# Optimization experiments

Measured on AMD Instinct MI355X. Metric: run time of the kernel, lower is better.

## Reference

```python
import jax, jax.numpy as jnp
import numpy as np

TAU = 0.5
EPS = 1e-8  # torch CosineSimilarity eps


def _normalize(v):
    # matches torch cosine sim: divide by max(||v||, eps)
    n = jnp.linalg.norm(v, axis=-1, keepdims=True)
    return v / jnp.maximum(n, EPS)


def setup_inputs() -> dict:
    key = jax.random.key(0)
    k1, k2 = jax.random.split(key)
    N, D = 4096, 256
    x = jax.random.normal(k1, (N, D), dtype=jnp.float32)
    y = jax.random.normal(k2, (N, D), dtype=jnp.float32)
    return {"x": x, "y": y}


def reference(x, y):
    n = x.shape[0]
    xn = _normalize(x)
    yn = _normalize(y)
    inv_tau = 1.0 / TAU
    sim_xx = (xn @ xn.T) * inv_tau  # [n, n]
    sim_yy = (yn @ yn.T) * inv_tau
    sim_xy = (xn @ yn.T) * inv_tau
    neg_inf = jnp.float32(-jnp.inf)
    diag = jnp.arange(n)
    sim_xx = sim_xx.at[diag, diag].set(neg_inf)
    sim_yy = sim_yy.at[diag, diag].set(neg_inf)
    scores1 = jnp.concatenate([sim_xy, sim_xx], axis=-1)          # [n, 2n]
    scores2 = jnp.concatenate([sim_yy, sim_xy.T], axis=-1)        # [n, 2n]
    scores = jnp.concatenate([scores1, scores2], axis=-2)          # [2n, 2n]
    targets = jnp.arange(2 * n)
    logp = jax.nn.log_softmax(scores, axis=-1)
    loss = -jnp.mean(logp[jnp.arange(2 * n), targets])
    return loss
```

## Files before the change

kernel.cpp:

```cpp
#include <hip/hip_runtime.h>
#include <hip/hip_bf16.h>


#define NROWS 8192
#define DDIM  256
#define BM    128
#define BN    64
#define COLSPLIT 8
#define COLS_PER (NROWS / COLSPLIT)
#define NT (COLS_PER / BN)

typedef __attribute__((ext_vector_type(8))) __bf16 bf16x8_t;
typedef __attribute__((ext_vector_type(4))) float  f32x4_t;

typedef __attribute__((address_space(1))) const void* as1_cvp;
typedef __attribute__((address_space(3))) void*       as3_vp;

#if __has_builtin(__builtin_amdgcn_exp2f)
#define EXP2F __builtin_amdgcn_exp2f
#else
#define EXP2F exp2f
#endif

#define TWO_LOG2E 2.8853900817779268f

__global__ __launch_bounds__(256) void normalize_diag_kernel(
    const float* __restrict__ x, const float* __restrict__ y,
    __hip_bfloat16* __restrict__ zb, float* __restrict__ rowdiag,
    float* __restrict__ rowsum) {
  const int g = blockIdx.x * 256 + threadIdx.x;
  if (g < NROWS) rowsum[g] = 0.f;

  const int w = threadIdx.x >> 6, lane = threadIdx.x & 63;
  const int i = blockIdx.x * 4 + w;
  const float4 xv = ((const float4*)(x + (size_t)i * DDIM))[lane];
  const float4 yv = ((const float4*)(y + (size_t)i * DDIM))[lane];
  float ssx = xv.x * xv.x + xv.y * xv.y + xv.z * xv.z + xv.w * xv.w;
  float ssy = yv.x * yv.x + yv.y * yv.y + yv.z * yv.z + yv.w * yv.w;
  float sxy = xv.x * yv.x + xv.y * yv.y + xv.z * yv.z + xv.w * yv.w;
  #pragma unroll
  for (int off = 32; off > 0; off >>= 1) {
    ssx += __shfl_xor(ssx, off, 64);
    ssy += __shfl_xor(ssy, off, 64);
    sxy += __shfl_xor(sxy, off, 64);
  }
  const float sclx = 1.0f / fmaxf(sqrtf(ssx), 1e-8f);
  const float scly = 1.0f / fmaxf(sqrtf(ssy), 1e-8f);
  __hip_bfloat16 px[4], py[4];
  px[0] = __float2bfloat16(xv.x * sclx); px[1] = __float2bfloat16(xv.y * sclx);
  px[2] = __float2bfloat16(xv.z * sclx); px[3] = __float2bfloat16(xv.w * sclx);
  py[0] = __float2bfloat16(yv.x * scly); py[1] = __float2bfloat16(yv.y * scly);
  py[2] = __float2bfloat16(yv.z * scly); py[3] = __float2bfloat16(yv.w * scly);
  *(short4*)(zb + (size_t)i * DDIM + lane * 4)            = *(short4*)px;
  *(short4*)(zb + (size_t)(i + 4096) * DDIM + lane * 4)   = *(short4*)py;
  if (lane == 0) rowdiag[i] = 2.0f * sxy * sclx * scly;
}

__global__ __launch_bounds__(512) void gram_lse_kernel(
    const __hip_bfloat16* __restrict__ zbh, float* __restrict__ rowsum) {
  __shared__ short smem[2][BN * DDIM];

  const short* zs = (const short*)zbh;
  const char* zbytes = (const char*)zs;
  const int tid  = threadIdx.x;
  const int w    = tid >> 6;
  const int lane = tid & 63;
  const int lhi  = lane >> 4;
  const int llo  = lane & 15;
  const int i0 = (blockIdx.x >> 3) * BM;
  const int c0 = (blockIdx.x & 7) * COLS_PER;
  const bool has_diag = ((blockIdx.x >> 6) == (blockIdx.x & 7));

  const int arow = i0 + w * 16 + llo;
  const float TBF = __bfloat162float(__float2bfloat16(TWO_LOG2E));
  bf16x8_t afrag[8];
  #pragma unroll
  for (int ks = 0; ks < 8; ++ks) {
    afrag[ks] = *(const bf16x8_t*)(zs + (size_t)arow * DDIM + ks * 32 + lhi * 8);
    #pragma unroll
    for (int e = 0; e < 8; ++e) {
      afrag[ks][e] = (__bf16)((float)afrag[ks][e] * TBF);
    }
  }

  size_t soff[4]; int loff[4];
  #pragma unroll
  for (int it = 0; it < 4; ++it) {
    const int o    = w * 4096 + it * 1024 + lane * 16;
    const int cr   = o >> 9;
    const int slot = (o >> 4) & 31;
    soff[it] = (size_t)cr * 512 + (size_t)((slot ^ (cr & 31)) << 4);
    loff[it] = w * 4096 + it * 1024;
  }

#define STAGE(buf, ct_) do {                                                  \
    const size_t cbase = (size_t)(c0 + (ct_) * BN) * 512;                     \
    _Pragma("unroll")                                                         \
    for (int it = 0; it < 4; ++it) {                                          \
      __builtin_amdgcn_global_load_lds(                                       \
          (as1_cvp)(zbytes + cbase + soff[it]),                               \
          (as3_vp)((char*)smem[buf] + loff[it]), 16, 0, 0);                   \
    }                                                                         \
  } while (0)

  float racc[4] = {0.f, 0.f, 0.f, 0.f};
  const int gr_base = i0 + w * 16 + lhi * 4;

  STAGE(0, 0);
  asm volatile("s_waitcnt vmcnt(0)" ::: "memory");
  __syncthreads();
  int cur = 0;

  for (int ct = 0; ct < NT; ++ct) {
    if (ct + 1 < NT) STAGE(cur ^ 1, ct + 1);
    const int cb = c0 + ct * BN;

    #pragma unroll
    for (int nt = 0; nt < 4; ++nt) {
      const int cr = nt * 16 + llo;
      f32x4_t acc = {0.f, 0.f, 0.f, 0.f};
      #pragma unroll
      for (int ks = 0; ks < 8; ++ks) {
        const int kg = ks * 4 + lhi;
        const bf16x8_t bfrag = *(const bf16x8_t*)(
            (const char*)smem[cur] + cr * 512 + ((kg ^ (cr & 31)) << 4));
        acc = __builtin_amdgcn_mfma_f32_16x16x32_bf16(afrag[ks], bfrag, acc, 0, 0, 0);
      }
      if (has_diag) {
        const int gc = cb + cr;
        #pragma unroll
        for (int j = 0; j < 4; ++j)
          racc[j] += ((gr_base + j) != gc) ? EXP2F(acc[j]) : 0.f;
      } else {
        #pragma unroll
        for (int j = 0; j < 4; ++j)
          racc[j] += EXP2F(acc[j]);
      }
    }
    asm volatile("s_waitcnt vmcnt(0)" ::: "memory");
    __syncthreads();
    cur ^= 1;
  }
#undef STAGE

  #pragma unroll
  for (int j = 0; j < 4; ++j) {
    float v = racc[j];
    v += __shfl_xor(v, 1, 16);
    v += __shfl_xor(v, 2, 16);
    v += __shfl_xor(v, 4, 16);
    v += __shfl_xor(v, 8, 16);
    if (llo == 0) atomicAdd(&rowsum[gr_base + j], v);
  }
}

__global__ __launch_bounds__(256) void finalize_kernel(
    const float* __restrict__ rowsum, const float* __restrict__ rowdiag,
    float* __restrict__ out) {
  const int t = threadIdx.x;
  float s = 0.f;
  for (int r4 = t; r4 < NROWS / 4; r4 += 256) {
    const float4 v = ((const float4*)rowsum)[r4];
    s += __logf(v.x) + __logf(v.y) + __logf(v.z) + __logf(v.w);
  }
  for (int i4 = t; i4 < 4096 / 4; i4 += 256) {
    const float4 d = ((const float4*)rowdiag)[i4];
    s -= 2.0f * (d.x + d.y + d.z + d.w);
  }
  #pragma unroll
  for (int off = 32; off > 0; off >>= 1) s += __shfl_xor(s, off, 64);
  __shared__ float wsum[4];
  const int w = t >> 6, lane = t & 63;
  if (lane == 0) wsum[w] = s;
  __syncthreads();
  if (t == 0) out[0] = (wsum[0] + wsum[1] + wsum[2] + wsum[3]) / (float)NROWS;
}

extern "C" void kernel_launch(void* const* d_in, const int* in_sizes, int n_in,
                              void* d_out, int out_size, void* d_ws, size_t ws_size,
                              hipStream_t stream) {
  const float* x = (const float*)d_in[0];
  const float* y = (const float*)d_in[1];
  float* out = (float*)d_out;

  char* ws = (char*)d_ws;
  __hip_bfloat16* zb = (__hip_bfloat16*)ws;
  float* rowsum  = (float*)(ws + (size_t)NROWS * DDIM * 2);
  float* rowdiag = rowsum + NROWS;

  normalize_diag_kernel<<<1024, 256, 0, stream>>>(x, y, zb, rowdiag, rowsum);
  gram_lse_kernel<<<512, 512, 0, stream>>>(zb, rowsum);
  finalize_kernel<<<1, 256, 0, stream>>>(rowsum, rowdiag, out);
}
```

Measured before the change: 55.35 us.

## Exploit Gram matrix symmetry by computing lower-triangular tiles only

```diff
diff --git a/kernel.cpp b/kernel.cpp
--- a/kernel.cpp
+++ b/kernel.cpp
@@ -6,9 +6,9 @@
 #define DDIM  256
 #define BM    128
 #define BN    64
-#define COLSPLIT 8
-#define COLS_PER (NROWS / COLSPLIT)
+#define COLS_PER 256
 #define NT (COLS_PER / BN)
+#define NBLK 1056
 
 typedef __attribute__((ext_vector_type(8))) __bf16 bf16x8_t;
 typedef __attribute__((ext_vector_type(4))) float  f32x4_t;
@@ -58,7 +58,8 @@
 
 __global__ __launch_bounds__(512) void gram_lse_kernel(
     const __hip_bfloat16* __restrict__ zbh, float* __restrict__ rowsum) {
-  __shared__ short smem[2][BN * DDIM];
+  __shared__ short smem[BN * DDIM];
+  __shared__ float colacc[COLS_PER];
 
   const short* zs = (const short*)zbh;
   const char* zbytes = (const char*)zs;
@@ -67,9 +68,15 @@
   const int lane = tid & 63;
   const int lhi  = lane >> 4;
   const int llo  = lane & 15;
-  const int i0 = (blockIdx.x >> 3) * BM;
-  const int c0 = (blockIdx.x & 7) * COLS_PER;
-  const bool has_diag = ((blockIdx.x >> 6) == (blockIdx.x & 7));
+
+  int jj = 0, rem = blockIdx.x;
+  while (rem >= 64 - 2 * jj) { rem -= 64 - 2 * jj; ++jj; }
+  const int I = 2 * jj + rem;
+  const int i0 = I * BM;
+  const int c0 = jj * COLS_PER;
+  const bool straddle = (rem <= 1);
+
+  if (tid < COLS_PER) colacc[tid] = 0.f;
 
   const int arow = i0 + w * 16 + llo;
   const float TBF = __bfloat162float(__float2bfloat16(TWO_LOG2E));
@@ -78,42 +85,36 @@
   for (int ks = 0; ks < 8; ++ks) {
     afrag[ks] = *(const bf16x8_t*)(zs + (size_t)arow * DDIM + ks * 32 + lhi * 8);
     #pragma unroll
-    for (int e = 0; e < 8; ++e) {
+    for (int e = 0; e < 8; ++e)
       afrag[ks][e] = (__bf16)((float)afrag[ks][e] * TBF);
-    }
   }
 
-  size_t soff[4]; int loff[4];
+  int soff[4], loff[4];
   #pragma unroll
   for (int it = 0; it < 4; ++it) {
-    const int o    = w * 4096 + it * 1024 + lane * 16;
+    const int o    = it * 8192 + tid * 16;
     const int cr   = o >> 9;
     const int slot = (o >> 4) & 31;
-    soff[it] = (size_t)cr * 512 + (size_t)((slot ^ (cr & 31)) << 4);
-    loff[it] = w * 4096 + it * 1024;
+    soff[it] = cr * 512 + ((slot ^ (cr & 31)) << 4);
+    loff[it] = it * 8192 + w * 1024;
   }
 
-#define STAGE(buf, ct_) do {                                                  \
-    const size_t cbase = (size_t)(c0 + (ct_) * BN) * 512;                     \
-    _Pragma("unroll")                                                         \
-    for (int it = 0; it < 4; ++it) {                                          \
-      __builtin_amdgcn_global_load_lds(                                       \
-          (as1_cvp)(zbytes + cbase + soff[it]),                               \
-          (as3_vp)((char*)smem[buf] + loff[it]), 16, 0, 0);                   \
-    }                                                                         \
-  } while (0)
-
   float racc[4] = {0.f, 0.f, 0.f, 0.f};
-  const int gr_base = i0 + w * 16 + lhi * 4;
-
-  STAGE(0, 0);
-  asm volatile("s_waitcnt vmcnt(0)" ::: "memory");
-  __syncthreads();
-  int cur = 0;
+  const int gr0 = i0 + w * 16 + lhi * 4;
 
   for (int ct = 0; ct < NT; ++ct) {
-    if (ct + 1 < NT) STAGE(cur ^ 1, ct + 1);
-    const int cb = c0 + ct * BN;
+    __syncthreads();
+    {
+      const size_t cbase = (size_t)(c0 + ct * BN) * 512;
+      #pragma unroll
+      for (int it = 0; it < 4; ++it) {
+        __builtin_amdgcn_global_load_lds(
+            (as1_cvp)(zbytes + cbase + (size_t)soff[it]),
+            (as3_vp)((char*)smem + loff[it]), 16, 0, 0);
+      }
+    }
+    asm volatile("s_waitcnt vmcnt(0)" ::: "memory");
+    __syncthreads();
 
     #pragma unroll
     for (int nt = 0; nt < 4; ++nt) {
@@ -123,25 +124,25 @@
       for (int ks = 0; ks < 8; ++ks) {
         const int kg = ks * 4 + lhi;
         const bf16x8_t bfrag = *(const bf16x8_t*)(
-            (const char*)smem[cur] + cr * 512 + ((kg ^ (cr & 31)) << 4));
+            (const char*)smem + cr * 512 + ((kg ^ (cr & 31)) << 4));
         acc = __builtin_amdgcn_mfma_f32_16x16x32_bf16(afrag[ks], bfrag, acc, 0, 0, 0);
       }
-      if (has_diag) {
-        const int gc = cb + cr;
+      const int gc = c0 + ct * BN + cr;
+      float e[4];
+      #pragma unroll
+      for (int j = 0; j < 4; ++j) e[j] = EXP2F(acc[j]);
+      if (straddle) {
         #pragma unroll
-        for (int j = 0; j < 4; ++j)
-          racc[j] += ((gr_base + j) != gc) ? EXP2F(acc[j]) : 0.f;
-      } else {
-        #pragma unroll
-        for (int j = 0; j < 4; ++j)
-          racc[j] += EXP2F(acc[j]);
+        for (int j = 0; j < 4; ++j) e[j] = ((gr0 + j) > gc) ? e[j] : 0.f;
       }
+      #pragma unroll
+      for (int j = 0; j < 4; ++j) racc[j] += e[j];
+      float cs = (e[0] + e[1]) + (e[2] + e[3]);
+      cs += __shfl_xor(cs, 16, 64);
+      cs += __shfl_xor(cs, 32, 64);
+      if (lane < 16) atomicAdd(&colacc[ct * BN + cr], cs);
     }
-    asm volatile("s_waitcnt vmcnt(0)" ::: "memory");
-    __syncthreads();
-    cur ^= 1;
   }
-#undef STAGE
 
   #pragma unroll
   for (int j = 0; j < 4; ++j) {
@@ -150,8 +151,11 @@
     v += __shfl_xor(v, 2, 16);
     v += __shfl_xor(v, 4, 16);
     v += __shfl_xor(v, 8, 16);
-    if (llo == 0) atomicAdd(&rowsum[gr_base + j], v);
+    if (llo == 0) atomicAdd(&rowsum[gr0 + j], v);
   }
+
+  __syncthreads();
+  if (tid < COLS_PER) atomicAdd(&rowsum[c0 + tid], colacc[tid]);
 }
 
 __global__ __launch_bounds__(256) void finalize_kernel(
@@ -189,6 +193,6 @@
   float* rowdiag = rowsum + NROWS;
 
   normalize_diag_kernel<<<1024, 256, 0, stream>>>(x, y, zb, rowdiag, rowsum);
-  gram_lse_kernel<<<512, 512, 0, stream>>>(zb, rowsum);
+  gram_lse_kernel<<<NBLK, 512, 0, stream>>>(zb, rowsum);
   finalize_kernel<<<1, 256, 0, stream>>>(rowsum, rowdiag, out);
 }
```

New measurement: 78.82 us. 1.42x slower.
